# Kernel optimization log

Measured on AMD Instinct MI355X. Metric: run time of the kernel, lower is better.

## Reference

```python
import jax, jax.numpy as jnp
import numpy as np

ROPE_THETA = 10000.0

def _rope(t):
    # t: (B, S, H, D) -- rotate-half RoPE over last dim
    B, S, H, D = t.shape
    inv_freq = 1.0 / (ROPE_THETA ** (jnp.arange(0, D, 2, dtype=jnp.float32) / D))  # (D/2,)
    ang = jnp.arange(S, dtype=jnp.float32)[:, None] * inv_freq[None, :]            # (S, D/2)
    cos = jnp.concatenate([jnp.cos(ang), jnp.cos(ang)], axis=-1)[None, :, None, :] # (1,S,1,D)
    sin = jnp.concatenate([jnp.sin(ang), jnp.sin(ang)], axis=-1)[None, :, None, :]
    t1, t2 = jnp.split(t, 2, axis=-1)
    rot = jnp.concatenate([-t2, t1], axis=-1)
    return t * cos.astype(t.dtype) + rot * sin.astype(t.dtype)

def setup_inputs() -> dict:
    key = jax.random.key(0)
    kx, kq, kk, kv, ko = jax.random.split(key, 5)
    B, S, DIM = 2, 2048, 2048
    x = jax.random.normal(kx, (B, S, DIM), dtype=jnp.float32)
    mask = jnp.tril(jnp.ones((S, S), dtype=bool))[None, None, :, :]  # causal (1,1,S,S)
    scale = DIM ** -0.5
    wq = jax.random.normal(kq, (DIM, DIM), dtype=jnp.float32) * scale
    wk = jax.random.normal(kk, (DIM, DIM), dtype=jnp.float32) * scale
    wv = jax.random.normal(kv, (DIM, DIM), dtype=jnp.float32) * scale
    wo = jax.random.normal(ko, (DIM, DIM), dtype=jnp.float32) * scale
    return {"x": x, "mask": mask, "wq": wq, "wk": wk, "wv": wv, "wo": wo}

def reference(x, mask, wq, wk, wv, wo):
    B, S, DIM = x.shape
    H = 16
    D = DIM // H
    scale = D ** -0.5
    # nn.Linear: y = x @ W.T
    q = (x @ wq.T).reshape(B, S, H, D)
    k = (x @ wk.T).reshape(B, S, H, D)
    v = (x @ wv.T).reshape(B, S, H, D)
    q = _rope(q)
    k = _rope(k)
    scores = jnp.einsum('bqhd,bkhd->bhqk', q, k) * scale
    scores = jnp.where(mask, scores, -jnp.inf)
    attn = jax.nn.softmax(scores, axis=-1)
    out = jnp.einsum('bhqk,bkhd->bqhd', attn, v).reshape(B, S, DIM)
    return out @ wo.T
```

## Files before the change

### kernel.cpp

```cpp
#include <hip/hip_runtime.h>
#include <cstdint>

typedef unsigned short u16;
typedef uint32_t u32;
typedef __attribute__((ext_vector_type(8))) short bf16x8;
typedef __attribute__((ext_vector_type(4))) float f32x4;
typedef __attribute__((ext_vector_type(16))) float f32x16;

#define DIM_ 2048
#define S_   2048
#define B_   2
#define H_   16
#define HD_  128
#define M_   (B_ * S_)

__device__ __forceinline__ u16 f2b(float f) {
  union { float f; uint32_t u; } v; v.f = f;
  uint32_t u = v.u;
  return (u16)((u + 0x7FFFu + ((u >> 16) & 1u)) >> 16);
}
__device__ __forceinline__ float b2f(u16 h) {
  union { uint32_t u; float f; } v; v.u = ((uint32_t)h) << 16;
  return v.f;
}

__device__ __forceinline__ u32 cvtpk(float lo, float hi) {
  u32 r;
  asm("v_cvt_pk_bf16_f32 %0, %1, %2" : "=v"(r) : "v"(lo), "v"(hi));
  return r;
}

typedef __attribute__((address_space(3))) u16 lds_u16_t;
typedef __attribute__((address_space(1))) const u16 glob_u16_t;

__device__ __forceinline__ void gload16(const u16* g, u16* l) {
  __builtin_amdgcn_global_load_lds((glob_u16_t*)g, (lds_u16_t*)l, 16, 0, 0);
}
#define GLD0(SRC, DST) \
  __builtin_amdgcn_global_load_lds((glob_u16_t*)(SRC), (lds_u16_t*)(DST), 16, 0, 0)

__global__ void convert5_kernel(const float* __restrict__ x, const float* __restrict__ wq,
                                const float* __restrict__ wk, const float* __restrict__ wv,
                                const float* __restrict__ wo, u16* __restrict__ xb,
                                u16* __restrict__ wqb, u16* __restrict__ wkb,
                                u16* __restrict__ wvb, u16* __restrict__ wob) {
  const float* src;
  u16* dst;
  int n;
  switch (blockIdx.y) {
    case 0: src = x;  dst = xb;  n = M_ * DIM_;   break;
    case 1: src = wq; dst = wqb; n = DIM_ * DIM_; break;
    case 2: src = wk; dst = wkb; n = DIM_ * DIM_; break;
    case 3: src = wv; dst = wvb; n = DIM_ * DIM_; break;
    default: src = wo; dst = wob; n = DIM_ * DIM_; break;
  }
  int i = (blockIdx.x * blockDim.x + threadIdx.x) * 4;
  const int stride = gridDim.x * blockDim.x * 4;
  for (; i < n; i += stride) {
    float4 v = *reinterpret_cast<const float4*>(src + i);
    uint64_t p = (uint64_t)f2b(v.x) | ((uint64_t)f2b(v.y) << 16) |
                 ((uint64_t)f2b(v.z) << 32) | ((uint64_t)f2b(v.w) << 48);
    *reinterpret_cast<uint64_t*>(dst + i) = p;
  }
}

__global__ void rope_table_kernel(float* __restrict__ cosT, float* __restrict__ sinT) {
  int i = blockIdx.x * blockDim.x + threadIdx.x;
  if (i >= S_ * 64) return;
  int s = i >> 6, d = i & 63;
  float inv = powf(10000.0f, -(float)d * (1.0f / 64.0f));
  float ang = (float)s * inv;
  cosT[i] = cosf(ang);
  sinT[i] = sinf(ang);
}

__global__ void rope_apply_kernel(u16* __restrict__ qb, u16* __restrict__ kb,
                                  const float* __restrict__ cosT,
                                  const float* __restrict__ sinT) {
  u16* buf = blockIdx.y ? kb : qb;
  int i = blockIdx.x * blockDim.x + threadIdx.x;
  if (i >= B_ * S_ * H_ * 8) return;
  const int c8 = i & 7;
  const int h = (i >> 3) & (H_ - 1);
  const int row = i >> 7;
  const int s = row & (S_ - 1);
  u16* p = buf + (size_t)row * DIM_ + h * HD_ + c8 * 8;
  bf16x8 t1v = *(bf16x8*)p;
  bf16x8 t2v = *(bf16x8*)(p + 64);
  const float4 c0 = *(const float4*)(cosT + s * 64 + c8 * 8);
  const float4 c1 = *(const float4*)(cosT + s * 64 + c8 * 8 + 4);
  const float4 s0 = *(const float4*)(sinT + s * 64 + c8 * 8);
  const float4 s1 = *(const float4*)(sinT + s * 64 + c8 * 8 + 4);
  const float cc[8] = {c0.x, c0.y, c0.z, c0.w, c1.x, c1.y, c1.z, c1.w};
  const float ss[8] = {s0.x, s0.y, s0.z, s0.w, s1.x, s1.y, s1.z, s1.w};
  bf16x8 o1, o2;
#pragma unroll
  for (int j = 0; j < 8; ++j) {
    const float t1 = b2f((u16)t1v[j]);
    const float t2 = b2f((u16)t2v[j]);
    o1[j] = (short)f2b(t1 * cc[j] - t2 * ss[j]);
    o2[j] = (short)f2b(t2 * cc[j] + t1 * ss[j]);
  }
  *(bf16x8*)p = o1;
  *(bf16x8*)(p + 64) = o2;
}

#define NT_ 32

#define LDA(DST, BASE)                                                         \
  _Pragma("unroll") for (int mi = 0; mi < 8; ++mi)                             \
      DST[mi] = *(const bf16x8*)((BASE) + mi * 1024);
#define LDB(DST, BASE)                                                         \
  _Pragma("unroll") for (int ni = 0; ni < NF_; ++ni)                           \
      DST[ni] = *(const bf16x8*)((BASE) + ni * 1024);

#define MFMA_KS(AV, BV)                                                        \
  _Pragma("unroll") for (int mi = 0; mi < 8; ++mi)                             \
    _Pragma("unroll") for (int ni = 0; ni < NF_; ++ni)                         \
        acc[mi][ni] = __builtin_amdgcn_mfma_f32_16x16x32_bf16(                 \
            AV[mi], BV[ni], acc[mi][ni], 0, 0, 0);

#define STAGE(BUF, OFFU) do {                                                  \
    _Pragma("unroll") for (int s = 0; s < ASW_; ++s)                           \
      GLD0(sA + goff + (OFFU) + s * (64 * DIM_),                               \
           lds + (BUF) * BUFSZ_ + s * 4096 + w * 512);                         \
    _Pragma("unroll") for (int s = 0; s < BSW_; ++s)                           \
      GLD0(sB + goff + (OFFU) + s * (64 * DIM_),                               \
           lds + (BUF) * BUFSZ_ + 16384 + s * 4096 + w * 512);                 \
  } while (0)

#define VMC_N() do {                                                           \
    if (ASW_ + BSW_ == 8) asm volatile("s_waitcnt vmcnt(8)" ::: "memory");     \
    else                  asm volatile("s_waitcnt vmcnt(6)" ::: "memory");     \
  } while (0)

#define TILE_N(BUF, NBUF, OFFU) do {                                           \
    LDA(a1, pAk1[BUF]); LDB(b1, pBk1[BUF]);                            \
    __builtin_amdgcn_sched_barrier(0);                                         \
    __builtin_amdgcn_s_setprio(1);                                             \
    MFMA_KS(a0, b0);                                                  \
    __builtin_amdgcn_s_setprio(0);                                             \
    asm volatile("s_waitcnt lgkmcnt(0)" ::: "memory");                         \
    __builtin_amdgcn_sched_barrier(0);                                         \
    __builtin_amdgcn_s_barrier();                                      \
    STAGE(BUF, OFFU);                                                          \
    __builtin_amdgcn_sched_barrier(0);                                         \
    VMC_N();                                                                   \
    __builtin_amdgcn_sched_barrier(0);                                         \
    __builtin_amdgcn_s_barrier();                                      \
    LDA(a0, pAk0[NBUF]); LDB(b0, pBk0[NBUF]);                          \
    __builtin_amdgcn_sched_barrier(0);                                         \
    __builtin_amdgcn_s_setprio(1);                                             \
    MFMA_KS(a1, b1);                                                  \
    __builtin_amdgcn_s_setprio(0);                                             \
  } while (0)

#define TILE_P(BUF, NBUF) do {                                   \
    LDA(a1, pAk1[BUF]); LDB(b1, pBk1[BUF]);                                    \
    __builtin_amdgcn_sched_barrier(0);                                         \
    __builtin_amdgcn_s_setprio(1);                                             \
    MFMA_KS(a0, b0);                                                           \
    __builtin_amdgcn_s_setprio(0);                                             \
    asm volatile("s_waitcnt lgkmcnt(0)" ::: "memory");                         \
    __builtin_amdgcn_sched_barrier(0);                                         \
    asm volatile("s_waitcnt vmcnt(0)" ::: "memory");                           \
    __builtin_amdgcn_sched_barrier(0);                                         \
    __builtin_amdgcn_s_barrier();                                              \
    LDA(a0, pAk0[NBUF]); LDB(b0, pBk0[NBUF]);                                  \
    __builtin_amdgcn_sched_barrier(0);                                         \
    __builtin_amdgcn_s_setprio(1);                                             \
    MFMA_KS(a1, b1);                                                           \
    __builtin_amdgcn_s_setprio(0);                                             \
  } while (0)

#define TILE_L(BUF) do {                                         \
    LDA(a1, pAk1[BUF]); LDB(b1, pBk1[BUF]);                                    \
    __builtin_amdgcn_sched_barrier(0);                                         \
    MFMA_KS(a0, b0);                                                           \
    MFMA_KS(a1, b1);                                                           \
  } while (0)

#define GEMM_V2_BODY(BN_)                                                      \
  constexpr int NF_ = (BN_) / 64;                                              \
  constexpr int ASW_ = 4;                                                      \
  constexpr int BSW_ = (BN_) / 64;                                             \
  constexpr int BUFSZ_ = 16384 + (BN_) * 64;                                   \
  const int tid = threadIdx.x;                                                 \
  const int lane = tid & 63;                                                   \
  const int w = tid >> 6;                                                      \
  const int wm = w >> 2, wn = w & 3;                                           \
  const int l15 = lane & 15, lg = lane >> 4;                                   \
  const int goff = (w * 8 + (lane >> 3)) * DIM_ + ((lane & 7) ^ (lane >> 3)) * 8; \
  const int x7 = l15 & 7;                                                      \
  const int lr0 = l15 * 64 + ((lg ^ x7) * 8);                                  \
  const int lr1 = l15 * 64 + (((4 | lg) ^ x7) * 8);                            \
  const u16* pAk0[2] = {lds + wm * 8192 + lr0, lds + BUFSZ_ + wm * 8192 + lr0};\
  const u16* pAk1[2] = {lds + wm * 8192 + lr1, lds + BUFSZ_ + wm * 8192 + lr1};\
  const u16* pBk0[2] = {lds + 16384 + wn * ((BN_)*16) + lr0,                   \
                        lds + BUFSZ_ + 16384 + wn * ((BN_)*16) + lr0};         \
  const u16* pBk1[2] = {lds + 16384 + wn * ((BN_)*16) + lr1,                   \
                        lds + BUFSZ_ + 16384 + wn * ((BN_)*16) + lr1};         \
  f32x4 acc[8][NF_];                                                           \
  _Pragma("unroll") for (int i = 0; i < 8; ++i)                                \
    _Pragma("unroll") for (int j = 0; j < NF_; ++j)                            \
        acc[i][j] = (f32x4){0.f, 0.f, 0.f, 0.f};                               \
  bf16x8 a0[8], a1[8], b0[NF_], b1[NF_];                                       \
  STAGE(0, 0);                                                                 \
  STAGE(1, 64);                                                                \
  __builtin_amdgcn_sched_barrier(0);                                           \
  VMC_N();                                                                     \
  __builtin_amdgcn_sched_barrier(0);                                           \
  __builtin_amdgcn_s_barrier();                                                \
  LDA(a0, pAk0[0]); LDB(b0, pBk0[0]);                                          \
  for (int t = 0; t < NT_ - 2; t += 2) {                                       \
    TILE_N(0, 1, 128);                                                         \
    TILE_N(1, 0, 192);                                                         \
    sA += 128; sB += 128;                                                      \
  }                                                                            \
  TILE_P(0, 1);                                                                \
  TILE_L(1);

__global__ __launch_bounds__(512, 2) void gemm256_qkv_kernel(
    const u16* __restrict__ xb, const u16* __restrict__ wqb, const u16* __restrict__ wkb,
    const u16* __restrict__ wvb, u16* __restrict__ qb, u16* __restrict__ kb,
    u16* __restrict__ vb) {
  __shared__ __align__(16) u16 lds[65536];

  const int bid = blockIdx.x;
  const int logical = (bid & 7) * 48 + (bid >> 3);
  const int mt = logical / 24;
  const int rem = logical % 24;
  const int z = rem >> 3;
  const int nt = rem & 7;
  const u16* Wm = (z == 0) ? wqb : (z == 1) ? wkb : wvb;
  u16* out = (z == 0) ? qb : (z == 1) ? kb : vb;

  const u16* sA = xb + (size_t)(mt * 256) * DIM_;
  const u16* sB = Wm + (size_t)(nt * 256) * DIM_;

  GEMM_V2_BODY(256)

#pragma unroll
  for (int mi = 0; mi < 8; ++mi)
#pragma unroll
    for (int ni = 0; ni < 4; ++ni) {
      const int row = mt * 256 + wm * 128 + mi * 16 + lg * 4;
      const int col = nt * 256 + wn * 64 + ni * 16 + l15;
#pragma unroll
      for (int r = 0; r < 4; ++r)
        out[(size_t)(row + r) * DIM_ + col] = f2b(acc[mi][ni][r]);
    }
}

__global__ __launch_bounds__(512, 2) void gemm_out_v2_kernel(const u16* __restrict__ A,
                                                             const u16* __restrict__ W,
                                                             float* __restrict__ Cf) {
  __shared__ __align__(16) u16 lds[49152];
  const int bid = blockIdx.x;
  const int logical = (bid & 7) * 32 + (bid >> 3);
  const int mt = logical >> 4;
  const int nt = logical & 15;

  const u16* sA = A + (size_t)(mt * 256) * DIM_;
  const u16* sB = W + (size_t)(nt * 128) * DIM_;

  GEMM_V2_BODY(128)

#pragma unroll
  for (int mi = 0; mi < 8; ++mi)
#pragma unroll
    for (int ni = 0; ni < 2; ++ni) {
      const int row = mt * 256 + wm * 128 + mi * 16 + lg * 4;
      const int col = nt * 128 + wn * 32 + ni * 16 + l15;
#pragma unroll
      for (int r = 0; r < 4; ++r)
        Cf[(size_t)(row + r) * DIM_ + col] = acc[mi][ni][r];
    }
}

#define CEXP 0.12751744f

__global__ __launch_bounds__(256, 2) void attn_kernel(const u16* __restrict__ q,
                                                      const u16* __restrict__ k,
                                                      const u16* __restrict__ v,
                                                      u16* __restrict__ ao) {
  __shared__ __align__(16) u16 smem[32768];
  u16* kTl = smem;
  u16* vTl = smem + 16384;

  const int qt   = blockIdx.z ? (int)blockIdx.x : (int)(gridDim.x - 1 - blockIdx.x);
  const int head = blockIdx.y;
  const int b    = blockIdx.z;
  const int t = threadIdx.x;
  const int lane = t & 63;
  const int w = t >> 6;
  const int l31 = lane & 31;
  const int hi = lane >> 5;
  const int kxor = (lane & 7) << 3;
  const int qrow0 = qt * 128 + w * 32;
  const size_t bS = (size_t)b * S_;

  bf16x8 qf[8];
  {
    const u16* qrow = q + (bS + qrow0 + l31) * DIM_ + head * HD_;
#pragma unroll
    for (int st = 0; st < 8; ++st)
      qf[st] = *(const bf16x8*)(qrow + st * 16 + hi * 8);
  }

  f32x16 accO[4];
#pragma unroll
  for (int db = 0; db < 4; ++db)
#pragma unroll
    for (int r = 0; r < 16; ++r) accO[db][r] = 0.f;
  float m = -1e30f, l = 0.f;

  const int tmax_w = 2 * qt + (w >> 1);
  const int ttend = 2 * qt + 1;

  bf16x8 vv[4];

  auto stageK = [&](int buf, int tt) {
#pragma unroll
    for (int p = 0; p < 4; ++p) {
      const int cid = p * 256 + w * 64 + lane;
      const int kr = cid >> 4;
      const int cg = (cid & 15) ^ (kr & 7);
      gload16(k + (bS + tt * 64 + kr) * DIM_ + head * HD_ + cg * 8,
              kTl + buf * 8192 + (p * 256 + w * 64) * 8);
    }
  };
  auto loadV = [&](int tt) {
#pragma unroll
    for (int p = 0; p < 4; ++p) {
      const int dchunk = p * 4 + w;
      vv[p] = *(const bf16x8*)(v + (bS + tt * 64 + lane) * DIM_ + head * HD_ + dchunk * 8);
    }
  };
  auto writeV = [&](int buf) {
#pragma unroll
    for (int p = 0; p < 4; ++p) {
      const int dchunk = p * 4 + w;
#pragma unroll
      for (int j = 0; j < 8; ++j) {
        const int d = dchunk * 8 + j;
        vTl[buf * 8192 + d * 64 + (lane ^ ((d & 7) << 3))] = (u16)vv[p][j];
      }
    }
  };

  stageK(0, 0);
  loadV(0);
  writeV(0);
  __syncthreads();

  for (int tt = 0; tt <= ttend; ++tt) {
    const int cur = tt & 1;
    const int alt = cur ^ 1;

    if (tt + 1 <= ttend) {
      stageK(alt, tt + 1);
      loadV(tt + 1);
    }

    if (tt <= tmax_w) {
      const u16* kB = kTl + cur * 8192;
      const u16* vB = vTl + cur * 8192;
      f32x16 sA, sB;
#pragma unroll
      for (int r = 0; r < 16; ++r) { sA[r] = 0.f; sB[r] = 0.f; }
      __builtin_amdgcn_s_setprio(1);
#pragma unroll
      for (int st = 0; st < 8; ++st) {
        const int dc = st * 16 + hi * 8;
        bf16x8 k0 = *(const bf16x8*)(kB + l31 * 128 + (dc ^ kxor));
        bf16x8 k1 = *(const bf16x8*)(kB + (32 + l31) * 128 + (dc ^ kxor));
        sA = __builtin_amdgcn_mfma_f32_32x32x16_bf16(k0, qf[st], sA, 0, 0, 0);
        sB = __builtin_amdgcn_mfma_f32_32x32x16_bf16(k1, qf[st], sB, 0, 0, 0);
      }
      __builtin_amdgcn_s_setprio(0);

      const int qg = qrow0 + l31;
      if (tt * 64 + 63 > qrow0) {
        const int kb = tt * 64 + 4 * hi;
#pragma unroll
        for (int r = 0; r < 16; ++r) {
          const int kg = kb + (r & 3) + 8 * (r >> 2);
          sA[r] = (kg <= qg) ? sA[r] : -1e30f;
          sB[r] = (kg + 32 <= qg) ? sB[r] : -1e30f;
        }
      }

      float mx[8];
#pragma unroll
      for (int i = 0; i < 8; ++i)
        mx[i] = fmaxf(fmaxf(sA[i], sA[i + 8]), fmaxf(sB[i], sB[i + 8]));
#pragma unroll
      for (int i = 0; i < 4; ++i) mx[i] = fmaxf(mx[i], mx[i + 4]);
      float pm = fmaxf(fmaxf(mx[0], mx[1]), fmaxf(mx[2], mx[3]));
      pm = fmaxf(pm, __shfl_xor(pm, 32));
      const float mN = fmaxf(m, pm);
      if (!__all(pm - m <= 90.5f)) {
        const float osc = exp2f((m - mN) * CEXP);
        l *= osc;
#pragma unroll
        for (int db = 0; db < 4; ++db)
#pragma unroll
          for (int r = 0; r < 16; ++r) accO[db][r] *= osc;
        m = mN;
      }
      const float mc = m * CEXP;
      float lsv[4] = {0.f, 0.f, 0.f, 0.f};
#pragma unroll
      for (int r = 0; r < 16; ++r) {
        const float pa = exp2f(__builtin_fmaf(sA[r], CEXP, -mc));
        const float pb = exp2f(__builtin_fmaf(sB[r], CEXP, -mc));
        sA[r] = pa; sB[r] = pb;
        lsv[r & 3] += pa + pb;
      }
      float ls = (lsv[0] + lsv[1]) + (lsv[2] + lsv[3]);
      ls += __shfl_xor(ls, 32);
      l += ls;

#define PV_STEP(ARR, R0, ST2)                                                      \
      {                                                                            \
        u32 a0 = cvtpk(ARR[(R0) + 0], ARR[(R0) + 1]);                              \
        u32 a1 = cvtpk(ARR[(R0) + 2], ARR[(R0) + 3]);                              \
        u32 b0 = cvtpk(ARR[(R0) + 4], ARR[(R0) + 5]);                              \
        u32 b1 = cvtpk(ARR[(R0) + 6], ARR[(R0) + 7]);                              \
        asm("v_permlane32_swap_b32 %0, %1" : "+v"(a0), "+v"(b0));                  \
        asm("v_permlane32_swap_b32 %0, %1" : "+v"(a1), "+v"(b1));                  \
        union { u32 uu[4]; bf16x8 v8; } pf;                                        \
        pf.uu[0] = a0; pf.uu[1] = a1; pf.uu[2] = b0; pf.uu[3] = b1;                \
        const int ko = (ST2) * 16 + hi * 8;                                        \
        __builtin_amdgcn_s_setprio(1);                                             \
        _Pragma("unroll")                                                          \
        for (int db = 0; db < 4; ++db) {                                           \
          const int dr = db * 32 + l31;                                            \
          bf16x8 vf = *(const bf16x8*)(vB + dr * 64 + (ko ^ kxor));                \
          accO[db] =                                                               \
              __builtin_amdgcn_mfma_f32_32x32x16_bf16(vf, pf.v8, accO[db], 0, 0, 0); \
        }                                                                          \
        __builtin_amdgcn_s_setprio(0);                                             \
      }
      PV_STEP(sA, 0, 0)
      PV_STEP(sA, 8, 1)
      PV_STEP(sB, 0, 2)
      PV_STEP(sB, 8, 3)
#undef PV_STEP
    }

    if (tt + 1 <= ttend) writeV(alt);
    __syncthreads();
  }

  const float linv = 1.0f / l;
  u16* oT = smem + w * 4352;
#pragma unroll
  for (int db = 0; db < 4; ++db)
#pragma unroll
    for (int q4 = 0; q4 < 4; ++q4) {
      const int dbase = db * 32 + q4 * 8 + hi * 4;
      const u32 lo = cvtpk(accO[db][q4 * 4 + 0] * linv, accO[db][q4 * 4 + 1] * linv);
      const u32 hiw = cvtpk(accO[db][q4 * 4 + 2] * linv, accO[db][q4 * 4 + 3] * linv);
      *(u32*)(oT + l31 * 136 + dbase) = lo;
      *(u32*)(oT + l31 * 136 + dbase + 2) = hiw;
    }
  __syncthreads();
#pragma unroll
  for (int i = 0; i < 8; ++i) {
    const int cid = i * 64 + lane;
    const int qloc = cid >> 4;
    const int c = cid & 15;
    const bf16x8 val = *(const bf16x8*)(oT + qloc * 136 + c * 8);
    *(bf16x8*)(ao + (bS + qrow0 + qloc) * DIM_ + head * HD_ + c * 8) = val;
  }
}

extern "C" void kernel_launch(void* const* d_in, const int* in_sizes, int n_in,
                              void* d_out, int out_size, void* d_ws, size_t ws_size,
                              hipStream_t stream) {
  const float* x  = (const float*)d_in[0];
  const float* wq = (const float*)d_in[2];
  const float* wk = (const float*)d_in[3];
  const float* wv = (const float*)d_in[4];
  const float* wo = (const float*)d_in[5];

  char* ws = (char*)d_ws;
  size_t off = 0;
  auto carve = [&](size_t bytes) { char* p = ws + off; off += bytes; return p; };
  u16* xb   = (u16*)carve((size_t)M_ * DIM_ * 2);
  u16* wqb  = (u16*)carve((size_t)DIM_ * DIM_ * 2);
  u16* wkb  = (u16*)carve((size_t)DIM_ * DIM_ * 2);
  u16* wvb  = (u16*)carve((size_t)DIM_ * DIM_ * 2);
  u16* wob  = (u16*)carve((size_t)DIM_ * DIM_ * 2);
  u16* qb   = (u16*)carve((size_t)M_ * DIM_ * 2);
  u16* kb   = (u16*)carve((size_t)M_ * DIM_ * 2);
  u16* vb   = (u16*)carve((size_t)M_ * DIM_ * 2);
  u16* aob  = (u16*)carve((size_t)M_ * DIM_ * 2);
  float* cosT = (float*)carve((size_t)S_ * 64 * 4);
  float* sinT = (float*)carve((size_t)S_ * 64 * 4);
  if (off > ws_size) return;

  dim3 gc(1024, 5);
  convert5_kernel<<<gc, 256, 0, stream>>>(x, wq, wk, wv, wo, xb, wqb, wkb, wvb, wob);
  rope_table_kernel<<<512, 256, 0, stream>>>(cosT, sinT);

  gemm256_qkv_kernel<<<384, 512, 0, stream>>>(xb, wqb, wkb, wvb, qb, kb, vb);

  dim3 gr((B_ * S_ * H_ * 8) / 256, 2);
  rope_apply_kernel<<<gr, 256, 0, stream>>>(qb, kb, cosT, sinT);

  dim3 ga(S_ / 128, H_, B_);
  attn_kernel<<<ga, 256, 0, stream>>>(qb, kb, vb, aob);

  gemm_out_v2_kernel<<<256, 512, 0, stream>>>(aob, wob, (float*)d_out);
}
```

Measured before the change: 277.9 us.

## Fuse RoPE into QKV GEMM epilogue and interleave attention grid by batch

Removes the separate RoPE pass over Q and K. The QKV GEMM now applies the rotation in its epilogue, using a permuted B-tile layout so that each wave holds both rotate-half partner columns in registers. This saves a full read and write of Q and K and one kernel launch, at the cost of scattered cos/sin table loads and strided bf16 stores in the epilogue. The attention grid is also flattened so both batches of a q-tile are scheduled together, heaviest tiles first, which may improve load balance across the causal workload.

```diff
diff --git a/kernel.cpp b/kernel.cpp
--- a/kernel.cpp
+++ b/kernel.cpp
@@ -74,37 +74,6 @@
   sinT[i] = sinf(ang);
 }
 
-__global__ void rope_apply_kernel(u16* __restrict__ qb, u16* __restrict__ kb,
-                                  const float* __restrict__ cosT,
-                                  const float* __restrict__ sinT) {
-  u16* buf = blockIdx.y ? kb : qb;
-  int i = blockIdx.x * blockDim.x + threadIdx.x;
-  if (i >= B_ * S_ * H_ * 8) return;
-  const int c8 = i & 7;
-  const int h = (i >> 3) & (H_ - 1);
-  const int row = i >> 7;
-  const int s = row & (S_ - 1);
-  u16* p = buf + (size_t)row * DIM_ + h * HD_ + c8 * 8;
-  bf16x8 t1v = *(bf16x8*)p;
-  bf16x8 t2v = *(bf16x8*)(p + 64);
-  const float4 c0 = *(const float4*)(cosT + s * 64 + c8 * 8);
-  const float4 c1 = *(const float4*)(cosT + s * 64 + c8 * 8 + 4);
-  const float4 s0 = *(const float4*)(sinT + s * 64 + c8 * 8);
-  const float4 s1 = *(const float4*)(sinT + s * 64 + c8 * 8 + 4);
-  const float cc[8] = {c0.x, c0.y, c0.z, c0.w, c1.x, c1.y, c1.z, c1.w};
-  const float ss[8] = {s0.x, s0.y, s0.z, s0.w, s1.x, s1.y, s1.z, s1.w};
-  bf16x8 o1, o2;
-#pragma unroll
-  for (int j = 0; j < 8; ++j) {
-    const float t1 = b2f((u16)t1v[j]);
-    const float t2 = b2f((u16)t2v[j]);
-    o1[j] = (short)f2b(t1 * cc[j] - t2 * ss[j]);
-    o2[j] = (short)f2b(t2 * cc[j] + t1 * ss[j]);
-  }
-  *(bf16x8*)p = o1;
-  *(bf16x8*)(p + 64) = o2;
-}
-
 #define NT_ 32
 
 #define LDA(DST, BASE)                                                         \
@@ -112,7 +81,8 @@
       DST[mi] = *(const bf16x8*)((BASE) + mi * 1024);
 #define LDB(DST, BASE)                                                         \
   _Pragma("unroll") for (int ni = 0; ni < NF_; ++ni)                           \
-      DST[ni] = *(const bf16x8*)((BASE) + ni * 1024);
+      DST[ni] = *(const bf16x8*)((BASE) +                                      \
+          (BPERM_ ? (((ni) & 1) * 1024 + ((ni) >> 1) * 4096) : (ni) * 1024));
 
 #define MFMA_KS(AV, BV)                                                        \
   _Pragma("unroll") for (int mi = 0; mi < 8; ++mi)                             \
@@ -180,8 +150,9 @@
     MFMA_KS(a1, b1);                                                           \
   } while (0)
 
-#define GEMM_V2_BODY(BN_)                                                      \
+#define GEMM_V2_BODY(BN_, BPERM__)                                             \
   constexpr int NF_ = (BN_) / 64;                                              \
+  constexpr int BPERM_ = (BPERM__);                                            \
   constexpr int ASW_ = 4;                                                      \
   constexpr int BSW_ = (BN_) / 64;                                             \
   constexpr int BUFSZ_ = 16384 + (BN_) * 64;                                   \
@@ -194,12 +165,14 @@
   const int x7 = l15 & 7;                                                      \
   const int lr0 = l15 * 64 + ((lg ^ x7) * 8);                                  \
   const int lr1 = l15 * 64 + (((4 | lg) ^ x7) * 8);                            \
+  const int bbase = BPERM_ ? ((wn >> 1) * 8192 + (wn & 1) * 2048)              \
+                           : (wn * ((BN_) * 16));                              \
   const u16* pAk0[2] = {lds + wm * 8192 + lr0, lds + BUFSZ_ + wm * 8192 + lr0};\
   const u16* pAk1[2] = {lds + wm * 8192 + lr1, lds + BUFSZ_ + wm * 8192 + lr1};\
-  const u16* pBk0[2] = {lds + 16384 + wn * ((BN_)*16) + lr0,                   \
-                        lds + BUFSZ_ + 16384 + wn * ((BN_)*16) + lr0};         \
-  const u16* pBk1[2] = {lds + 16384 + wn * ((BN_)*16) + lr1,                   \
-                        lds + BUFSZ_ + 16384 + wn * ((BN_)*16) + lr1};         \
+  const u16* pBk0[2] = {lds + 16384 + bbase + lr0,                             \
+                        lds + BUFSZ_ + 16384 + bbase + lr0};                   \
+  const u16* pBk1[2] = {lds + 16384 + bbase + lr1,                             \
+                        lds + BUFSZ_ + 16384 + bbase + lr1};                   \
   f32x4 acc[8][NF_];                                                           \
   _Pragma("unroll") for (int i = 0; i < 8; ++i)                                \
     _Pragma("unroll") for (int j = 0; j < NF_; ++j)                            \
@@ -223,7 +196,7 @@
 __global__ __launch_bounds__(512, 2) void gemm256_qkv_kernel(
     const u16* __restrict__ xb, const u16* __restrict__ wqb, const u16* __restrict__ wkb,
     const u16* __restrict__ wvb, u16* __restrict__ qb, u16* __restrict__ kb,
-    u16* __restrict__ vb) {
+    u16* __restrict__ vb, const float* __restrict__ cosT, const float* __restrict__ sinT) {
   __shared__ __align__(16) u16 lds[65536];
 
   const int bid = blockIdx.x;
@@ -238,18 +211,41 @@
   const u16* sA = xb + (size_t)(mt * 256) * DIM_;
   const u16* sB = Wm + (size_t)(nt * 256) * DIM_;
 
-  GEMM_V2_BODY(256)
-
-#pragma unroll
-  for (int mi = 0; mi < 8; ++mi)
-#pragma unroll
-    for (int ni = 0; ni < 4; ++ni) {
+  GEMM_V2_BODY(256, 1)
+
+  const int colbase = nt * 256 + (wn >> 1) * 128 + (wn & 1) * 32;
+  if (z < 2) {
+#pragma unroll
+    for (int mi = 0; mi < 8; ++mi) {
       const int row = mt * 256 + wm * 128 + mi * 16 + lg * 4;
-      const int col = nt * 256 + wn * 64 + ni * 16 + l15;
-#pragma unroll
-      for (int r = 0; r < 4; ++r)
-        out[(size_t)(row + r) * DIM_ + col] = f2b(acc[mi][ni][r]);
-    }
+#pragma unroll
+      for (int r = 0; r < 4; ++r) {
+        const int s = (row + r) & (S_ - 1);
+#pragma unroll
+        for (int ni = 0; ni < 2; ++ni) {
+          const int d = (wn & 1) * 32 + ni * 16 + l15;
+          const float c  = cosT[s * 64 + d];
+          const float sn = sinT[s * 64 + d];
+          const float t1 = acc[mi][ni][r];
+          const float t2 = acc[mi][ni + 2][r];
+          u16* p = out + (size_t)(row + r) * DIM_ + colbase + ni * 16 + l15;
+          p[0]  = f2b(t1 * c - t2 * sn);
+          p[64] = f2b(t2 * c + t1 * sn);
+        }
+      }
+    }
+  } else {
+#pragma unroll
+    for (int mi = 0; mi < 8; ++mi)
+#pragma unroll
+      for (int ni = 0; ni < 4; ++ni) {
+        const int row = mt * 256 + wm * 128 + mi * 16 + lg * 4;
+        const int col = colbase + (ni & 1) * 16 + (ni >> 1) * 64 + l15;
+#pragma unroll
+        for (int r = 0; r < 4; ++r)
+          out[(size_t)(row + r) * DIM_ + col] = f2b(acc[mi][ni][r]);
+      }
+  }
 }
 
 __global__ __launch_bounds__(512, 2) void gemm_out_v2_kernel(const u16* __restrict__ A,
@@ -264,7 +260,7 @@
   const u16* sA = A + (size_t)(mt * 256) * DIM_;
   const u16* sB = W + (size_t)(nt * 128) * DIM_;
 
-  GEMM_V2_BODY(128)
+  GEMM_V2_BODY(128, 0)
 
 #pragma unroll
   for (int mi = 0; mi < 8; ++mi)
@@ -288,9 +284,10 @@
   u16* kTl = smem;
   u16* vTl = smem + 16384;
 
-  const int qt   = blockIdx.z ? (int)blockIdx.x : (int)(gridDim.x - 1 - blockIdx.x);
+  const int r_    = blockIdx.x;
+  const int qt   = 15 - (r_ >> 1);
+  const int b    = r_ & 1;
   const int head = blockIdx.y;
-  const int b    = blockIdx.z;
   const int t = threadIdx.x;
   const int lane = t & 63;
   const int w = t >> 6;
@@ -312,7 +309,7 @@
 #pragma unroll
   for (int db = 0; db < 4; ++db)
 #pragma unroll
-    for (int r = 0; r < 16; ++r) accO[db][r] = 0.f;
+    for (int rr = 0; rr < 16; ++rr) accO[db][rr] = 0.f;
   float m = -1e30f, l = 0.f;
 
   const int tmax_w = 2 * qt + (w >> 1);
@@ -368,7 +365,7 @@
       const u16* vB = vTl + cur * 8192;
       f32x16 sA, sB;
 #pragma unroll
-      for (int r = 0; r < 16; ++r) { sA[r] = 0.f; sB[r] = 0.f; }
+      for (int rr = 0; rr < 16; ++rr) { sA[rr] = 0.f; sB[rr] = 0.f; }
       __builtin_amdgcn_s_setprio(1);
 #pragma unroll
       for (int st = 0; st < 8; ++st) {
@@ -384,10 +381,10 @@
       if (tt * 64 + 63 > qrow0) {
         const int kb = tt * 64 + 4 * hi;
 #pragma unroll
-        for (int r = 0; r < 16; ++r) {
-          const int kg = kb + (r & 3) + 8 * (r >> 2);
-          sA[r] = (kg <= qg) ? sA[r] : -1e30f;
-          sB[r] = (kg + 32 <= qg) ? sB[r] : -1e30f;
+        for (int rr = 0; rr < 16; ++rr) {
+          const int kg = kb + (rr & 3) + 8 * (rr >> 2);
+          sA[rr] = (kg <= qg) ? sA[rr] : -1e30f;
+          sB[rr] = (kg + 32 <= qg) ? sB[rr] : -1e30f;
         }
       }
 
@@ -406,17 +403,17 @@
 #pragma unroll
         for (int db = 0; db < 4; ++db)
 #pragma unroll
-          for (int r = 0; r < 16; ++r) accO[db][r] *= osc;
+          for (int rr = 0; rr < 16; ++rr) accO[db][rr] *= osc;
         m = mN;
       }
       const float mc = m * CEXP;
       float lsv[4] = {0.f, 0.f, 0.f, 0.f};
 #pragma unroll
-      for (int r = 0; r < 16; ++r) {
-        const float pa = exp2f(__builtin_fmaf(sA[r], CEXP, -mc));
-        const float pb = exp2f(__builtin_fmaf(sB[r], CEXP, -mc));
-        sA[r] = pa; sB[r] = pb;
-        lsv[r & 3] += pa + pb;
+      for (int rr = 0; rr < 16; ++rr) {
+        const float pa = exp2f(__builtin_fmaf(sA[rr], CEXP, -mc));
+        const float pb = exp2f(__builtin_fmaf(sB[rr], CEXP, -mc));
+        sA[rr] = pa; sB[rr] = pb;
+        lsv[rr & 3] += pa + pb;
       }
       float ls = (lsv[0] + lsv[1]) + (lsv[2] + lsv[3]);
       ls += __shfl_xor(ls, 32);
@@ -506,12 +503,9 @@
   convert5_kernel<<<gc, 256, 0, stream>>>(x, wq, wk, wv, wo, xb, wqb, wkb, wvb, wob);
   rope_table_kernel<<<512, 256, 0, stream>>>(cosT, sinT);
 
-  gemm256_qkv_kernel<<<384, 512, 0, stream>>>(xb, wqb, wkb, wvb, qb, kb, vb);
-
-  dim3 gr((B_ * S_ * H_ * 8) / 256, 2);
-  rope_apply_kernel<<<gr, 256, 0, stream>>>(qb, kb, cosT, sinT);
-
-  dim3 ga(S_ / 128, H_, B_);
+  gemm256_qkv_kernel<<<384, 512, 0, stream>>>(xb, wqb, wkb, wvb, qb, kb, vb, cosT, sinT);
+
+  dim3 ga(32, H_);
   attn_kernel<<<ga, 256, 0, stream>>>(qb, kb, vb, aob);
 
   gemm_out_v2_kernel<<<256, 512, 0, stream>>>(aob, wob, (float*)d_out);
```

After: 280.8 us. About the same (+1.0%).
